# Optimization experiments

Measured on AMD Instinct MI355X. Metric: run time of the kernel, lower is better.

The kernel has to match this reference:

```python
import jax, jax.numpy as jnp
import numpy as np

B, C, H, W = 4, 128, 64, 64
CI = C // 2  # inter_channels
BN_EPS = 1e-5


def _conv1x1(x, w, b):
    # x: [B,C,H,W], w: [O,C], b: [O] -> [B,O,H,W]
    return jnp.einsum('bchw,oc->bohw', x, w) + b[None, :, None, None]


def setup_inputs() -> dict:
    key = jax.random.key(0)
    ks = jax.random.split(key, 11)
    s_in = 1.0 / np.sqrt(C)
    s_mid = 1.0 / np.sqrt(CI)
    return {
        'x': jax.random.normal(ks[0], (B, C, H, W), dtype=jnp.float32),
        'g_w': jax.random.normal(ks[1], (CI, C), dtype=jnp.float32) * s_in,
        'g_b': jax.random.normal(ks[2], (CI,), dtype=jnp.float32) * 0.01,
        'theta_w': jax.random.normal(ks[3], (CI, C), dtype=jnp.float32) * s_in,
        'theta_b': jax.random.normal(ks[4], (CI,), dtype=jnp.float32) * 0.01,
        'phi_w': jax.random.normal(ks[5], (CI, C), dtype=jnp.float32) * s_in,
        'phi_b': jax.random.normal(ks[6], (CI,), dtype=jnp.float32) * 0.01,
        'w_w': jax.random.normal(ks[7], (C, CI), dtype=jnp.float32) * s_mid,
        'w_b': jax.random.normal(ks[8], (C,), dtype=jnp.float32) * 0.01,
        'bn_gamma': jnp.ones((C,), dtype=jnp.float32),
        'bn_beta': jnp.zeros((C,), dtype=jnp.float32),
    }


def reference(x, g_w, g_b, theta_w, theta_b, phi_w, phi_b, w_w, w_b, bn_gamma, bn_beta):
    b, c, h, w = x.shape
    n = h * w
    # 1x1 conv projections, flattened over spatial positions -> [B,N,CI]
    g_x = _conv1x1(x, g_w, g_b).reshape(b, CI, n).transpose(0, 2, 1)
    theta_x = _conv1x1(x, theta_w, theta_b).reshape(b, CI, n).transpose(0, 2, 1)
    phi_x = _conv1x1(x, phi_w, phi_b).reshape(b, CI, n)  # [B,CI,N]
    # full attention over spatial tokens: [B,N,N]
    f = jnp.einsum('bnc,bcm->bnm', theta_x, phi_x)
    f_div_c = jax.nn.softmax(f, axis=-1)
    y = jnp.einsum('bnm,bmc->bnc', f_div_c, g_x)  # [B,N,CI]
    y = y.transpose(0, 2, 1).reshape(b, CI, h, w)
    w_y = _conv1x1(y, w_w, w_b)  # [B,C,H,W]
    # BatchNorm2d (training-mode batch statistics over B,H,W)
    mean = jnp.mean(w_y, axis=(0, 2, 3))
    var = jnp.var(w_y, axis=(0, 2, 3))
    bn = bn_gamma[None, :, None, None] * (w_y - mean[None, :, None, None]) \
         * jax.lax.rsqrt(var + BN_EPS)[None, :, None, None] + bn_beta[None, :, None, None]
    return bn + x
```

## Files before the change

### kernel.cpp

```cpp
#include <hip/hip_runtime.h>
#include <math.h>

#define NSP 4096
#define CC  128
#define CIC 64
#define NB  4
#define LOG2E 1.4426950408889634f

typedef unsigned short u16;
typedef short s8bf __attribute__((ext_vector_type(8)));
typedef float f32x4 __attribute__((ext_vector_type(4)));
typedef float f32x2 __attribute__((ext_vector_type(2)));

#define MFMA(a, b, c) __builtin_amdgcn_mfma_f32_16x16x32_bf16(a, b, c, 0, 0, 0)

#define WSB_PB    0
#define WSB_PH    (NB * CC * NSP * 2)
#define WSB_Y     (WSB_PH + NB * NSP * CIC * 2)
#define WSB_WT4   (WSB_Y + NB * CIC * NSP * 4)
#define WSB_WT2P  (WSB_WT4 + CC * 256 * 4)
#define WSB_PARTS (WSB_WT2P + CIC * CC * 4)

__device__ __forceinline__ u16 f2bf(float f) {
    union { float f; unsigned u; } v; v.f = f;
    unsigned r = v.u + 0x7fffu + ((v.u >> 16) & 1u);
    return (u16)(r >> 16);
}

__global__ __launch_bounds__(256) void prep_kernel(
    const float* __restrict__ g_w, const float* __restrict__ t_w,
    const float* __restrict__ p_w, const float* __restrict__ w_w,
    float* __restrict__ wT4, float* __restrict__ wT2p)
{
    const int c = blockIdx.x;
    const int o = threadIdx.x;
    if (o < 192) {
        float v;
        if (o < 64)       v = g_w[o * CC + c];
        else if (o < 128) v = t_w[(o - 64) * CC + c] * LOG2E;
        else              v = p_w[(o - 128) * CC + c];
        wT4[(c << 8) + ((o & 63) << 2) + (o >> 6)] = v;
    } else {
        wT4[(c << 8) + ((o - 192) << 2) + 3] = 0.f;
    }
    if (o < CIC)
        wT2p[(o << 7) + ((c & 63) << 1) + (c >> 6)] = w_w[c * CIC + o];
}

__global__ __launch_bounds__(512) void proj_kernel(
    const float* __restrict__ x, const float* __restrict__ wT4,
    const float* __restrict__ g_b, const float* __restrict__ t_b,
    const float* __restrict__ p_b,
    u16* __restrict__ PB, u16* __restrict__ ph_tm)
{
    __shared__ float Xs[CC][36];
    __shared__ u16 Ot[192][40];

    const int b    = blockIdx.y;
    const int n0   = blockIdx.x * 32;
    const int tid  = threadIdx.x;
    const int lane = tid & 63;
    const int wv   = tid >> 6;
    const int t0   = wv * 4;

    const float* xb = x + (size_t)b * CC * NSP + n0;
    #pragma unroll
    for (int k = 0; k < 2; ++k) {
        int idx = tid + (k << 9);
        int c = idx >> 3, t4 = (idx & 7) << 2;
        *(f32x4*)&Xs[c][t4] = *(const f32x4*)(xb + (size_t)c * NSP + t4);
    }
    __syncthreads();

    float acc[3][4];
    {
        float b0 = g_b[lane], b1 = t_b[lane] * LOG2E, b2 = p_b[lane];
        #pragma unroll
        for (int t = 0; t < 4; ++t) { acc[0][t] = b0; acc[1][t] = b1; acc[2][t] = b2; }
    }

    const float* wp = wT4 + (lane << 2);
    #pragma unroll 8
    for (int c = 0; c < CC; ++c) {
        f32x4 wv4 = *(const f32x4*)(wp + (c << 8));
        f32x4 xv  = *(const f32x4*)&Xs[c][t0];
        #pragma unroll
        for (int t = 0; t < 4; ++t) {
            acc[0][t] += wv4[0] * xv[t];
            acc[1][t] += wv4[1] * xv[t];
            acc[2][t] += wv4[2] * xv[t];
        }
    }

    #pragma unroll
    for (int p = 0; p < 3; ++p) {
        #pragma unroll
        for (int i = 0; i < 2; ++i) {
            unsigned pk = (unsigned)f2bf(acc[p][2 * i]) | ((unsigned)f2bf(acc[p][2 * i + 1]) << 16);
            *(unsigned*)&Ot[lane + 64 * p][t0 + 2 * i] = pk;
        }
    }
    __syncthreads();

    {
        int row = tid >> 2, ch = tid & 3;
        uint4 v = *(const uint4*)&Ot[row][ch * 8];
        *(uint4*)(PB + (size_t)b * CC * NSP + (size_t)row * NSP + n0 + ch * 8) = v;
    }
    if (tid < 256) {
        int t = tid >> 3, c8 = (tid & 7) * 8;
        union { u16 tmp[8]; uint4 v4; } u;
        #pragma unroll
        for (int j = 0; j < 8; ++j) u.tmp[j] = Ot[128 + c8 + j][t];
        *(uint4*)(ph_tm + ((size_t)b * NSP + n0 + t) * 64 + c8) = u.v4;
    }
}

__global__ __launch_bounds__(512, 2) void attn_kernel(
    const u16* __restrict__ PB, const u16* __restrict__ ph_tm,
    float* __restrict__ y)
{
    const int b    = blockIdx.y;
    const int q0   = blockIdx.x << 6;
    const int tid  = threadIdx.x;
    const int lane = tid & 63;
    const int w    = tid >> 6;
    const int s    = w & 3;
    const int h    = w >> 2;
    const int l15  = lane & 15;
    const int g16  = lane >> 4;

    __shared__ __align__(16) char KV[2][2][2][8192];
    __shared__ __align__(16) u16 Plds[8][16][80];
    __shared__ float Om[4][16][68];
    __shared__ float Lm[4][16];

    const u16* gp  = PB + (size_t)b * CC * NSP;
    const u16* thc = gp + (size_t)CIC * NSP;
    const u16* php = ph_tm + (size_t)b * NSP * 64;

    const int srow = tid >> 3;
    const int scol = tid & 7;
    const int ldst = srow * 128 + (((scol ^ (srow & 7)) & 7) << 4);

    float4 rK0, rK1, rV0, rV1;
    auto load_t = [&](int t) {
        const int m0 = t << 6;
        rK0 = *(const float4*)(php + ((size_t)(       m0 + srow) << 6) + (scol << 3));
        rK1 = *(const float4*)(php + ((size_t)(2048 + m0 + srow) << 6) + (scol << 3));
        rV0 = *(const float4*)(gp + (size_t)srow * NSP +        m0 + (scol << 3));
        rV1 = *(const float4*)(gp + (size_t)srow * NSP + 2048 + m0 + (scol << 3));
    };
    auto write_t = [&](int buf) {
        *(float4*)(&KV[buf][0][0][0] + ldst) = rK0;
        *(float4*)(&KV[buf][0][1][0] + ldst) = rK1;
        *(float4*)(&KV[buf][1][0][0] + ldst) = rV0;
        *(float4*)(&KV[buf][1][1][0] + ldst) = rV1;
    };

    s8bf qa0, qa1;
    const int qtok = q0 + s * 16 + l15;
    #pragma unroll
    for (int j = 0; j < 8; ++j) {
        qa0[j] = (short)thc[(size_t)(g16 * 8 + j) * NSP + qtok];
        qa1[j] = (short)thc[(size_t)(32 + g16 * 8 + j) * NSP + qtok];
    }

    const s8bf ones = {0x3F80, 0x3F80, 0x3F80, 0x3F80, 0x3F80, 0x3F80, 0x3F80, 0x3F80};
    const f32x4 cinit = {-32.f, -32.f, -32.f, -32.f};

    f32x4 Ov[4];
    f32x4 lr = (f32x4){0.f, 0.f, 0.f, 0.f};
    #pragma unroll
    for (int c = 0; c < 4; ++c) Ov[c] = (f32x4){0.f, 0.f, 0.f, 0.f};

    load_t(0); write_t(0); load_t(1);
    __syncthreads();

    const int pin    = l15 & 7;
    const int pchb   = l15 >> 3;
    const int rmask  = (g16 ^ ((l15 >> 1) & 7)) << 3;
    const int rmask1 = ((4 + g16) ^ ((l15 >> 1) & 7)) << 3;

    for (int t = 0; t < 32; ++t) {
        const int buf = t & 1;
        const char* Kb = &KV[buf][0][h][0];
        const char* Vb = &KV[buf][1][h][0];

        f32x4 sv[4];
        __builtin_amdgcn_s_setprio(1);
        #pragma unroll
        for (int c = 0; c < 4; ++c) {
            const int tok = c * 16 + l15;
            const int sx  = (tok & 7) << 4;
            s8bf k0 = *(const s8bf*)(Kb + tok * 128 + ((g16 * 16)      ^ sx));
            s8bf k1 = *(const s8bf*)(Kb + tok * 128 + ((g16 * 16 + 64) ^ sx));
            sv[c] = MFMA(qa0, k0, cinit);
            sv[c] = MFMA(qa1, k1, sv[c]);
        }
        __builtin_amdgcn_s_setprio(0);

        u16 (&Pl)[16][80] = Plds[w];
        #pragma unroll
        for (int c = 0; c < 4; ++c) {
            #pragma unroll
            for (int r = 0; r < 4; ++r) {
                const int row = g16 * 4 + r;
                const int swc = ((c * 2 + pchb) ^ ((row >> 1) & 7)) << 3;
                Pl[row][swc | pin] = f2bf(__builtin_amdgcn_exp2f(sv[c][r]));
            }
        }

        s8bf pa0 = *(const s8bf*)&Pl[l15][rmask];
        s8bf pa1 = *(const s8bf*)&Pl[l15][rmask1];
        __builtin_amdgcn_s_setprio(1);
        lr = MFMA(pa0, ones, lr);
        lr = MFMA(pa1, ones, lr);
        #pragma unroll
        for (int c = 0; c < 4; ++c) {
            const int ci = c * 16 + l15;
            const int sx = (ci & 7) << 4;
            s8bf v0 = *(const s8bf*)(Vb + ci * 128 + ((g16 * 16)      ^ sx));
            s8bf v1 = *(const s8bf*)(Vb + ci * 128 + ((g16 * 16 + 64) ^ sx));
            Ov[c] = MFMA(pa0, v0, Ov[c]);
            Ov[c] = MFMA(pa1, v1, Ov[c]);
        }
        __builtin_amdgcn_s_setprio(0);

        if (t < 31) {
            write_t(buf ^ 1);
            if (t < 30) load_t(t + 2);
        }
        __syncthreads();
    }

    if (h == 1) {
        #pragma unroll
        for (int c = 0; c < 4; ++c) {
            #pragma unroll
            for (int r = 0; r < 4; ++r)
                Om[s][g16 * 4 + r][c * 16 + l15] = Ov[c][r];
        }
        if (l15 == 0) {
            #pragma unroll
            for (int r = 0; r < 4; ++r) Lm[s][g16 * 4 + r] = lr[r];
        }
    }
    __syncthreads();
    if (h == 0) {
        float inv[4];
        #pragma unroll
        for (int r = 0; r < 4; ++r) inv[r] = 1.0f / (lr[r] + Lm[s][g16 * 4 + r]);
        #pragma unroll
        for (int c = 0; c < 4; ++c) {
            #pragma unroll
            for (int r = 0; r < 4; ++r) {
                int row = g16 * 4 + r, col = c * 16 + l15;
                Om[s][row][col] = (Ov[c][r] + Om[s][row][col]) * inv[r];
            }
        }
    }
    __syncthreads();

    #pragma unroll
    for (int k = 0; k < 2; ++k) {
        int idx = tid + (k << 9);
        int ci = idx >> 4, q4 = (idx & 15) << 2;
        int ss = q4 >> 4, r0 = q4 & 15;
        float4 v;
        v.x = Om[ss][r0][ci]; v.y = Om[ss][r0 + 1][ci];
        v.z = Om[ss][r0 + 2][ci]; v.w = Om[ss][r0 + 3][ci];
        *(float4*)&y[((size_t)b * CIC + ci) * NSP + q0 + q4] = v;
    }
}

__global__ __launch_bounds__(256) void wconv_kernel(
    const float* __restrict__ y, const float* __restrict__ wT2p,
    const float* __restrict__ w_b, float* __restrict__ out)
{
    __shared__ float Ys[CIC][36];
    __shared__ float Of[CC][36];

    const int b    = blockIdx.y;
    const int n0   = blockIdx.x * 32;
    const int tid  = threadIdx.x;
    const int lane = tid & 63;
    const int wv   = tid >> 6;
    const int t0   = wv * 8;

    const float* yb = y + (size_t)b * CIC * NSP + n0;
    #pragma unroll
    for (int k = 0; k < 2; ++k) {
        int idx = tid + (k << 8);
        int c = idx >> 3, t4 = (idx & 7) << 2;
        *(f32x4*)&Ys[c][t4] = *(const f32x4*)(yb + (size_t)c * NSP + t4);
    }
    __syncthreads();

    float acc[2][8];
    #pragma unroll
    for (int t = 0; t < 8; ++t) { acc[0][t] = 0.f; acc[1][t] = 0.f; }

    const float* wp = wT2p + (lane << 1);
    #pragma unroll 8
    for (int ci = 0; ci < CIC; ++ci) {
        f32x2 wv2 = *(const f32x2*)(wp + (ci << 7));
        f32x4 y0 = *(const f32x4*)&Ys[ci][t0];
        f32x4 y1 = *(const f32x4*)&Ys[ci][t0 + 4];
        #pragma unroll
        for (int t = 0; t < 4; ++t) {
            acc[0][t]     += wv2[0] * y0[t];
            acc[0][4 + t] += wv2[0] * y1[t];
            acc[1][t]     += wv2[1] * y0[t];
            acc[1][4 + t] += wv2[1] * y1[t];
        }
    }

    float b0 = w_b[lane], b1 = w_b[64 + lane];
    #pragma unroll
    for (int t = 0; t < 4; ++t) {
        Of[lane][t0 + t]          = acc[0][t] + b0;
        Of[lane][t0 + 4 + t]      = acc[0][4 + t] + b0;
        Of[64 + lane][t0 + t]     = acc[1][t] + b1;
        Of[64 + lane][t0 + 4 + t] = acc[1][4 + t] + b1;
    }
    __syncthreads();

    float* ob = out + (size_t)b * CC * NSP + n0;
    #pragma unroll
    for (int k = 0; k < 4; ++k) {
        int idx = tid + (k << 8);
        int row = idx >> 3, ch = idx & 7;
        *(float4*)(ob + (size_t)row * NSP + ch * 4) = *(const float4*)&Of[row][ch * 4];
    }
}

__global__ __launch_bounds__(256) void stats_kernel(
    const float* __restrict__ wy, float* __restrict__ parts)
{
    const int c   = blockIdx.x >> 2;
    const int qd  = blockIdx.x & 3;
    const int tid = threadIdx.x;
    float s = 0.f, ss = 0.f;
    #pragma unroll 4
    for (int k = 0; k < 16; ++k) {
        int i = qd * 4096 + k * 256 + tid;
        int b = i >> 12, n = i & (NSP - 1);
        float v = wy[((size_t)b * CC + c) * NSP + n];
        s += v; ss += v * v;
    }
    #pragma unroll
    for (int off = 32; off > 0; off >>= 1) {
        s  += __shfl_down(s, off, 64);
        ss += __shfl_down(ss, off, 64);
    }
    __shared__ float sred[4], ssred[4];
    const int wid = tid >> 6, lane = tid & 63;
    if (lane == 0) { sred[wid] = s; ssred[wid] = ss; }
    __syncthreads();
    if (tid == 0) {
        parts[(c * 4 + qd) * 2]     = sred[0] + sred[1] + sred[2] + sred[3];
        parts[(c * 4 + qd) * 2 + 1] = ssred[0] + ssred[1] + ssred[2] + ssred[3];
    }
}

__global__ __launch_bounds__(256) void bn_kernel(
    const float* __restrict__ x, const float* __restrict__ parts,
    const float* __restrict__ gamma, const float* __restrict__ beta,
    float* __restrict__ out)
{
    const int i = blockIdx.x * 256 + threadIdx.x;
    const int c = (i >> 10) & (CC - 1);
    float s  = parts[c * 8]     + parts[c * 8 + 2] + parts[c * 8 + 4] + parts[c * 8 + 6];
    float ss = parts[c * 8 + 1] + parts[c * 8 + 3] + parts[c * 8 + 5] + parts[c * 8 + 7];
    float mean = s * (1.0f / 16384.0f);
    float var  = ss * (1.0f / 16384.0f) - mean * mean;
    float istd = rsqrtf(var + 1e-5f);
    float ga = gamma[c] * istd;
    float be = beta[c] - mean * ga;
    float4 wy = ((const float4*)out)[i];
    float4 xv = ((const float4*)x)[i];
    float4 o;
    o.x = wy.x * ga + be + xv.x;
    o.y = wy.y * ga + be + xv.y;
    o.z = wy.z * ga + be + xv.z;
    o.w = wy.w * ga + be + xv.w;
    ((float4*)out)[i] = o;
}

extern "C" void kernel_launch(void* const* d_in, const int* in_sizes, int n_in,
                              void* d_out, int out_size, void* d_ws, size_t ws_size,
                              hipStream_t stream)
{
    const float* x    = (const float*)d_in[0];
    const float* g_w  = (const float*)d_in[1];
    const float* g_b  = (const float*)d_in[2];
    const float* t_w  = (const float*)d_in[3];
    const float* t_b  = (const float*)d_in[4];
    const float* p_w  = (const float*)d_in[5];
    const float* p_b  = (const float*)d_in[6];
    const float* w_w  = (const float*)d_in[7];
    const float* w_b  = (const float*)d_in[8];
    const float* bn_g = (const float*)d_in[9];
    const float* bn_b = (const float*)d_in[10];
    float* out = (float*)d_out;
    char* ws8  = (char*)d_ws;

    u16*   PB    = (u16*)(ws8 + WSB_PB);
    u16*   PH    = (u16*)(ws8 + WSB_PH);
    float* y     = (float*)(ws8 + WSB_Y);
    float* wT4   = (float*)(ws8 + WSB_WT4);
    float* wT2p  = (float*)(ws8 + WSB_WT2P);
    float* parts = (float*)(ws8 + WSB_PARTS);

    prep_kernel <<<dim3(CC), 256, 0, stream>>>(g_w, t_w, p_w, w_w, wT4, wT2p);
    proj_kernel <<<dim3(NSP / 32, NB), 512, 0, stream>>>(x, wT4, g_b, t_b, p_b, PB, PH);
    attn_kernel <<<dim3(NSP / 64, NB), 512, 0, stream>>>(PB, PH, y);
    wconv_kernel<<<dim3(NSP / 32, NB), 256, 0, stream>>>(y, wT2p, w_b, out);
    stats_kernel<<<dim3(CC * 4), 256, 0, stream>>>(out, parts);
    bn_kernel   <<<dim3(2048), 256, 0, stream>>>(x, parts, bn_g, bn_b, out);
}
```

Measured before the change: 78.81 us.

## Split KV across blocks with 32x32 MFMA attention and register-resident P

Rewrites the attention kernel to use 32x32x16 bf16 MFMA with 128-query tiles and splits the KV range into four chunks across a new grid dimension. Each chunk writes unnormalized partial outputs and row sums, which the wconv kernel merges and normalizes. P is kept in registers and rearranged with cross-lane shuffles instead of a round trip through LDS, and row sums become plain adds instead of extra MFMAs. The aim is more parallel blocks and fewer LDS and MFMA instructions per tile. In exchange it adds global traffic for the fp32 partial outputs and an extra reduction in wconv.

```diff
diff --git a/kernel.cpp b/kernel.cpp
--- a/kernel.cpp
+++ b/kernel.cpp
@@ -1,4 +1,5 @@
 #include <hip/hip_runtime.h>
+#include <hip/hip_bf16.h>
 #include <math.h>
 
 #define NSP 4096
@@ -8,16 +9,20 @@
 #define LOG2E 1.4426950408889634f
 
 typedef unsigned short u16;
+typedef unsigned int u32;
 typedef short s8bf __attribute__((ext_vector_type(8)));
 typedef float f32x4 __attribute__((ext_vector_type(4)));
 typedef float f32x2 __attribute__((ext_vector_type(2)));
-
-#define MFMA(a, b, c) __builtin_amdgcn_mfma_f32_16x16x32_bf16(a, b, c, 0, 0, 0)
+typedef float f32x16 __attribute__((ext_vector_type(16)));
+
+#define MFMA32(a, b, c) __builtin_amdgcn_mfma_f32_32x32x16_bf16(a, b, c, 0, 0, 0)
 
 #define WSB_PB    0
-#define WSB_PH    (NB * CC * NSP * 2)
-#define WSB_Y     (WSB_PH + NB * NSP * CIC * 2)
-#define WSB_WT4   (WSB_Y + NB * CIC * NSP * 4)
+#define WSB_TH    (NB * CIC * NSP * 2)
+#define WSB_PH    (WSB_TH + NB * NSP * CIC * 2)
+#define WSB_OP    (WSB_PH + NB * NSP * CIC * 2)
+#define WSB_LP    (WSB_OP + (size_t)NB * 4 * NSP * CIC * 4)
+#define WSB_WT4   (WSB_LP + NB * 4 * NSP * 4)
 #define WSB_WT2P  (WSB_WT4 + CC * 256 * 4)
 #define WSB_PARTS (WSB_WT2P + CIC * CC * 4)
 
@@ -51,7 +56,7 @@
     const float* __restrict__ x, const float* __restrict__ wT4,
     const float* __restrict__ g_b, const float* __restrict__ t_b,
     const float* __restrict__ p_b,
-    u16* __restrict__ PB, u16* __restrict__ ph_tm)
+    u16* __restrict__ PB, u16* __restrict__ th_tm, u16* __restrict__ ph_tm)
 {
     __shared__ float Xs[CC][36];
     __shared__ u16 Ot[192][40];
@@ -102,42 +107,44 @@
     }
     __syncthreads();
 
-    {
+    if (tid < 256) {
         int row = tid >> 2, ch = tid & 3;
         uint4 v = *(const uint4*)&Ot[row][ch * 8];
-        *(uint4*)(PB + (size_t)b * CC * NSP + (size_t)row * NSP + n0 + ch * 8) = v;
-    }
-    if (tid < 256) {
-        int t = tid >> 3, c8 = (tid & 7) * 8;
-        union { u16 tmp[8]; uint4 v4; } u;
-        #pragma unroll
-        for (int j = 0; j < 8; ++j) u.tmp[j] = Ot[128 + c8 + j][t];
-        *(uint4*)(ph_tm + ((size_t)b * NSP + n0 + t) * 64 + c8) = u.v4;
-    }
-}
-
-__global__ __launch_bounds__(512, 2) void attn_kernel(
-    const u16* __restrict__ PB, const u16* __restrict__ ph_tm,
-    float* __restrict__ y)
-{
-    const int b    = blockIdx.y;
-    const int q0   = blockIdx.x << 6;
+        *(uint4*)(PB + (size_t)b * CIC * NSP + (size_t)row * NSP + n0 + ch * 8) = v;
+    }
+    {
+        int tok = tid >> 4, sel = (tid >> 3) & 1, c8 = (tid & 7) * 8;
+        u16* dst = (sel ? ph_tm : th_tm) + ((size_t)b * NSP + n0 + tok) * 64 + c8;
+        union { u16 t[8]; uint4 v4; } u;
+        #pragma unroll
+        for (int j = 0; j < 8; ++j) u.t[j] = Ot[64 + sel * 64 + c8 + j][tok];
+        *(uint4*)dst = u.v4;
+    }
+}
+
+__global__ __launch_bounds__(512, 4) void attn_kernel(
+    const u16* __restrict__ PB, const u16* __restrict__ th_tm,
+    const u16* __restrict__ ph_tm,
+    float* __restrict__ O_part, float* __restrict__ l_part)
+{
+    const int b    = blockIdx.z;
+    const int kvs  = blockIdx.y;
+    const int q0   = blockIdx.x << 7;
     const int tid  = threadIdx.x;
     const int lane = tid & 63;
     const int w    = tid >> 6;
     const int s    = w & 3;
     const int h    = w >> 2;
-    const int l15  = lane & 15;
-    const int g16  = lane >> 4;
+    const int l31  = lane & 31;
+    const int l5   = lane >> 5;
 
     __shared__ __align__(16) char KV[2][2][2][8192];
-    __shared__ __align__(16) u16 Plds[8][16][80];
-    __shared__ float Om[4][16][68];
-    __shared__ float Lm[4][16];
-
-    const u16* gp  = PB + (size_t)b * CC * NSP;
-    const u16* thc = gp + (size_t)CIC * NSP;
-    const u16* php = ph_tm + (size_t)b * NSP * 64;
+
+    const u16* gp = PB + (size_t)b * CIC * NSP;
+    const u16* th = th_tm + (size_t)b * NSP * 64;
+    const u16* ph = ph_tm + (size_t)b * NSP * 64;
+
+    const int kb0 = kvs << 10;
 
     const int srow = tid >> 3;
     const int scol = tid & 7;
@@ -145,11 +152,11 @@
 
     float4 rK0, rK1, rV0, rV1;
     auto load_t = [&](int t) {
-        const int m0 = t << 6;
-        rK0 = *(const float4*)(php + ((size_t)(       m0 + srow) << 6) + (scol << 3));
-        rK1 = *(const float4*)(php + ((size_t)(2048 + m0 + srow) << 6) + (scol << 3));
-        rV0 = *(const float4*)(gp + (size_t)srow * NSP +        m0 + (scol << 3));
-        rV1 = *(const float4*)(gp + (size_t)srow * NSP + 2048 + m0 + (scol << 3));
+        const int m0 = kb0 + (t << 6);
+        rK0 = *(const float4*)(ph + ((size_t)(m0 + srow) << 6) + (scol << 3));
+        rK1 = *(const float4*)(ph + ((size_t)(m0 + 512 + srow) << 6) + (scol << 3));
+        rV0 = *(const float4*)(gp + (size_t)srow * NSP + m0 + (scol << 3));
+        rV1 = *(const float4*)(gp + (size_t)srow * NSP + m0 + 512 + (scol << 3));
     };
     auto write_t = [&](int buf) {
         *(float4*)(&KV[buf][0][0][0] + ldst) = rK0;
@@ -158,125 +165,120 @@
         *(float4*)(&KV[buf][1][1][0] + ldst) = rV1;
     };
 
-    s8bf qa0, qa1;
-    const int qtok = q0 + s * 16 + l15;
-    #pragma unroll
-    for (int j = 0; j < 8; ++j) {
-        qa0[j] = (short)thc[(size_t)(g16 * 8 + j) * NSP + qtok];
-        qa1[j] = (short)thc[(size_t)(32 + g16 * 8 + j) * NSP + qtok];
-    }
-
-    const s8bf ones = {0x3F80, 0x3F80, 0x3F80, 0x3F80, 0x3F80, 0x3F80, 0x3F80, 0x3F80};
-    const f32x4 cinit = {-32.f, -32.f, -32.f, -32.f};
-
-    f32x4 Ov[4];
-    f32x4 lr = (f32x4){0.f, 0.f, 0.f, 0.f};
-    #pragma unroll
-    for (int c = 0; c < 4; ++c) Ov[c] = (f32x4){0.f, 0.f, 0.f, 0.f};
+    s8bf qb[4];
+    const int qtok = q0 + (s << 5) + l31;
+    #pragma unroll
+    for (int fc = 0; fc < 4; ++fc)
+        qb[fc] = *(const s8bf*)(th + ((size_t)qtok << 6) + fc * 16 + l5 * 8);
+
+    f32x16 Ov0, Ov1, cinit;
+    #pragma unroll
+    for (int i = 0; i < 16; ++i) { Ov0[i] = 0.f; Ov1[i] = 0.f; cinit[i] = -32.f; }
+    float lr = 0.f;
 
     load_t(0); write_t(0); load_t(1);
     __syncthreads();
 
-    const int pin    = l15 & 7;
-    const int pchb   = l15 >> 3;
-    const int rmask  = (g16 ^ ((l15 >> 1) & 7)) << 3;
-    const int rmask1 = ((4 + g16) ^ ((l15 >> 1) & 7)) << 3;
-
-    for (int t = 0; t < 32; ++t) {
+    u32 pk[2][4][2];
+
+    for (int t = 0; t < 8; ++t) {
         const int buf = t & 1;
         const char* Kb = &KV[buf][0][h][0];
         const char* Vb = &KV[buf][1][h][0];
 
-        f32x4 sv[4];
+        #pragma unroll
+        for (int kt = 0; kt < 2; ++kt) {
+            const int trow = l31 + (kt << 5);
+            const int rswz = trow & 7;
+            f32x16 sv = cinit;
+            __builtin_amdgcn_s_setprio(1);
+            #pragma unroll
+            for (int fc = 0; fc < 4; ++fc) {
+                s8bf ka = *(const s8bf*)(Kb + trow * 128 + (((2 * fc + l5) ^ rswz) << 4));
+                sv = MFMA32(ka, qb[fc], sv);
+            }
+            __builtin_amdgcn_s_setprio(0);
+            float e[16];
+            #pragma unroll
+            for (int i = 0; i < 16; ++i) e[i] = __builtin_amdgcn_exp2f(sv[i]);
+            #pragma unroll
+            for (int i = 0; i < 16; ++i) lr += e[i];
+            #pragma unroll
+            for (int m = 0; m < 4; ++m) {
+                #pragma unroll
+                for (int i = 0; i < 2; ++i) {
+                    __hip_bfloat162 hh = __float22bfloat162_rn(
+                        make_float2(e[4 * m + 2 * i], e[4 * m + 2 * i + 1]));
+                    union { __hip_bfloat162 h2; u32 u; } cv; cv.h2 = hh;
+                    pk[kt][m][i] = cv.u;
+                }
+            }
+        }
+
         __builtin_amdgcn_s_setprio(1);
         #pragma unroll
-        for (int c = 0; c < 4; ++c) {
-            const int tok = c * 16 + l15;
-            const int sx  = (tok & 7) << 4;
-            s8bf k0 = *(const s8bf*)(Kb + tok * 128 + ((g16 * 16)      ^ sx));
-            s8bf k1 = *(const s8bf*)(Kb + tok * 128 + ((g16 * 16 + 64) ^ sx));
-            sv[c] = MFMA(qa0, k0, cinit);
-            sv[c] = MFMA(qa1, k1, sv[c]);
+        for (int f = 0; f < 4; ++f) {
+            const int tt = f >> 1;
+            const int m0c = 2 * (f & 1);
+            u32 sA0 = pk[tt][m0c][0],     sA1 = pk[tt][m0c][1];
+            u32 sB0 = pk[tt][m0c + 1][0], sB1 = pk[tt][m0c + 1][1];
+            u32 self0 = l5 ? sB0 : sA0, self1 = l5 ? sB1 : sA1;
+            u32 send0 = l5 ? sA0 : sB0, send1 = l5 ? sA1 : sB1;
+            u32 x0 = (u32)__shfl_xor((int)send0, 32);
+            u32 x1 = (u32)__shfl_xor((int)send1, 32);
+            union { u32 u[4]; s8bf v; } pa;
+            pa.u[0] = l5 ? x0 : self0;
+            pa.u[1] = l5 ? x1 : self1;
+            pa.u[2] = l5 ? self0 : x0;
+            pa.u[3] = l5 ? self1 : x1;
+            const int c1 = l31 + 32;
+            s8bf v0 = *(const s8bf*)(Vb + l31 * 128 + (((2 * f + l5) ^ (l31 & 7)) << 4));
+            s8bf v1 = *(const s8bf*)(Vb + c1 * 128 + (((2 * f + l5) ^ (c1 & 7)) << 4));
+            Ov0 = MFMA32(pa.v, v0, Ov0);
+            Ov1 = MFMA32(pa.v, v1, Ov1);
         }
         __builtin_amdgcn_s_setprio(0);
 
-        u16 (&Pl)[16][80] = Plds[w];
-        #pragma unroll
-        for (int c = 0; c < 4; ++c) {
-            #pragma unroll
-            for (int r = 0; r < 4; ++r) {
-                const int row = g16 * 4 + r;
-                const int swc = ((c * 2 + pchb) ^ ((row >> 1) & 7)) << 3;
-                Pl[row][swc | pin] = f2bf(__builtin_amdgcn_exp2f(sv[c][r]));
-            }
-        }
-
-        s8bf pa0 = *(const s8bf*)&Pl[l15][rmask];
-        s8bf pa1 = *(const s8bf*)&Pl[l15][rmask1];
-        __builtin_amdgcn_s_setprio(1);
-        lr = MFMA(pa0, ones, lr);
-        lr = MFMA(pa1, ones, lr);
-        #pragma unroll
-        for (int c = 0; c < 4; ++c) {
-            const int ci = c * 16 + l15;
-            const int sx = (ci & 7) << 4;
-            s8bf v0 = *(const s8bf*)(Vb + ci * 128 + ((g16 * 16)      ^ sx));
-            s8bf v1 = *(const s8bf*)(Vb + ci * 128 + ((g16 * 16 + 64) ^ sx));
-            Ov[c] = MFMA(pa0, v0, Ov[c]);
-            Ov[c] = MFMA(pa1, v1, Ov[c]);
-        }
-        __builtin_amdgcn_s_setprio(0);
-
-        if (t < 31) {
+        if (t < 7) {
             write_t(buf ^ 1);
-            if (t < 30) load_t(t + 2);
+            if (t < 6) load_t(t + 2);
         }
         __syncthreads();
     }
 
+    float lrh = lr + __shfl_xor(lr, 32);
+    float* Olds = (float*)&KV[0][0][0][0];
+    float* Llds = (float*)&KV[1][0][0][0];
+
     if (h == 1) {
         #pragma unroll
-        for (int c = 0; c < 4; ++c) {
-            #pragma unroll
-            for (int r = 0; r < 4; ++r)
-                Om[s][g16 * 4 + r][c * 16 + l15] = Ov[c][r];
-        }
-        if (l15 == 0) {
-            #pragma unroll
-            for (int r = 0; r < 4; ++r) Lm[s][g16 * 4 + r] = lr[r];
-        }
+        for (int reg = 0; reg < 16; ++reg) {
+            int q = (reg & 3) + 8 * (reg >> 2) + 4 * l5;
+            Olds[((s << 5) + q) * 64 + l31]      = Ov0[reg];
+            Olds[((s << 5) + q) * 64 + 32 + l31] = Ov1[reg];
+        }
+        if (l5 == 0) Llds[(s << 5) + l31] = lrh;
     }
     __syncthreads();
     if (h == 0) {
-        float inv[4];
-        #pragma unroll
-        for (int r = 0; r < 4; ++r) inv[r] = 1.0f / (lr[r] + Lm[s][g16 * 4 + r]);
-        #pragma unroll
-        for (int c = 0; c < 4; ++c) {
-            #pragma unroll
-            for (int r = 0; r < 4; ++r) {
-                int row = g16 * 4 + r, col = c * 16 + l15;
-                Om[s][row][col] = (Ov[c][r] + Om[s][row][col]) * inv[r];
-            }
-        }
-    }
-    __syncthreads();
-
-    #pragma unroll
-    for (int k = 0; k < 2; ++k) {
-        int idx = tid + (k << 9);
-        int ci = idx >> 4, q4 = (idx & 15) << 2;
-        int ss = q4 >> 4, r0 = q4 & 15;
-        float4 v;
-        v.x = Om[ss][r0][ci]; v.y = Om[ss][r0 + 1][ci];
-        v.z = Om[ss][r0 + 2][ci]; v.w = Om[ss][r0 + 3][ci];
-        *(float4*)&y[((size_t)b * CIC + ci) * NSP + q0 + q4] = v;
+        float ltot = lrh + Llds[(s << 5) + l31];
+        float* Ob = O_part + ((size_t)b * 4 + kvs) * NSP * 64;
+        #pragma unroll
+        for (int reg = 0; reg < 16; ++reg) {
+            int q = (reg & 3) + 8 * (reg >> 2) + 4 * l5;
+            int qg = q0 + (s << 5) + q;
+            Ob[(size_t)qg * 64 + l31]      = Ov0[reg] + Olds[((s << 5) + q) * 64 + l31];
+            Ob[(size_t)qg * 64 + 32 + l31] = Ov1[reg] + Olds[((s << 5) + q) * 64 + 32 + l31];
+        }
+        if (l5 == 0)
+            l_part[((size_t)b * 4 + kvs) * NSP + q0 + (s << 5) + l31] = ltot;
     }
 }
 
 __global__ __launch_bounds__(256) void wconv_kernel(
-    const float* __restrict__ y, const float* __restrict__ wT2p,
-    const float* __restrict__ w_b, float* __restrict__ out)
+    const float* __restrict__ O_part, const float* __restrict__ l_part,
+    const float* __restrict__ wT2p, const float* __restrict__ w_b,
+    float* __restrict__ out)
 {
     __shared__ float Ys[CIC][36];
     __shared__ float Of[CC][36];
@@ -288,12 +290,21 @@
     const int wv   = tid >> 6;
     const int t0   = wv * 8;
 
-    const float* yb = y + (size_t)b * CIC * NSP + n0;
-    #pragma unroll
-    for (int k = 0; k < 2; ++k) {
-        int idx = tid + (k << 8);
-        int c = idx >> 3, t4 = (idx & 7) << 2;
-        *(f32x4*)&Ys[c][t4] = *(const f32x4*)(yb + (size_t)c * NSP + t4);
+    #pragma unroll
+    for (int rnd = 0; rnd < 2; ++rnd) {
+        int tok = (tid >> 4) + (rnd << 4);
+        int ci4 = tid & 15;
+        int qg  = n0 + tok;
+        f32x4 a = {0.f, 0.f, 0.f, 0.f};
+        float ls = 0.f;
+        #pragma unroll
+        for (int kvs = 0; kvs < 4; ++kvs) {
+            a += *(const f32x4*)(O_part + (((size_t)b * 4 + kvs) * NSP + qg) * 64 + (ci4 << 2));
+            ls += l_part[((size_t)b * 4 + kvs) * NSP + qg];
+        }
+        float inv = 1.0f / ls;
+        #pragma unroll
+        for (int j = 0; j < 4; ++j) Ys[(ci4 << 2) + j][tok] = a[j] * inv;
     }
     __syncthreads();
 
@@ -407,16 +418,18 @@
     char* ws8  = (char*)d_ws;
 
     u16*   PB    = (u16*)(ws8 + WSB_PB);
+    u16*   TH    = (u16*)(ws8 + WSB_TH);
     u16*   PH    = (u16*)(ws8 + WSB_PH);
-    float* y     = (float*)(ws8 + WSB_Y);
+    float* OP    = (float*)(ws8 + WSB_OP);
+    float* LP    = (float*)(ws8 + WSB_LP);
     float* wT4   = (float*)(ws8 + WSB_WT4);
     float* wT2p  = (float*)(ws8 + WSB_WT2P);
     float* parts = (float*)(ws8 + WSB_PARTS);
 
     prep_kernel <<<dim3(CC), 256, 0, stream>>>(g_w, t_w, p_w, w_w, wT4, wT2p);
-    proj_kernel <<<dim3(NSP / 32, NB), 512, 0, stream>>>(x, wT4, g_b, t_b, p_b, PB, PH);
-    attn_kernel <<<dim3(NSP / 64, NB), 512, 0, stream>>>(PB, PH, y);
-    wconv_kernel<<<dim3(NSP / 32, NB), 256, 0, stream>>>(y, wT2p, w_b, out);
+    proj_kernel <<<dim3(NSP / 32, NB), 512, 0, stream>>>(x, wT4, g_b, t_b, p_b, PB, TH, PH);
+    attn_kernel <<<dim3(NSP / 128, 4, NB), 512, 0, stream>>>(PB, TH, PH, OP, LP);
+    wconv_kernel<<<dim3(NSP / 32, NB), 256, 0, stream>>>(OP, LP, wT2p, w_b, out);
     stats_kernel<<<dim3(CC * 4), 256, 0, stream>>>(out, parts);
     bn_kernel   <<<dim3(2048), 256, 0, stream>>>(x, parts, bn_g, bn_b, out);
 }
```

After: 80.53 us. +2.2%, slower.
